# Performance work log

Measured on AMD Instinct MI355X. Metric: run time of the kernel, lower is better.

## Reference

```python
import jax, jax.numpy as jnp
import numpy as np

N = 40000       # nodes
E = 400000      # directed edges (before self-loops)
F_IN = 50       # PPI num_features
HID = 64        # per-head hidden
H = 4           # heads
NCLS = 121      # PPI num_classes
NEG_SLOPE = 0.2


def gat_layer(x, src, dst, W, a_src, a_dst, W_res, b, concat):
    """PyG GATConv: per-edge attention, segment softmax over dst, scatter-add."""
    n = x.shape[0]
    h, c = a_src.shape
    feat = (x @ W).reshape(n, h, c)                       # [N,H,C]
    al_s = (feat * a_src[None]).sum(-1)                   # [N,H]
    al_d = (feat * a_dst[None]).sum(-1)                   # [N,H]
    e = jax.nn.leaky_relu(al_s[src] + al_d[dst], NEG_SLOPE)  # [E,H]
    m = jax.ops.segment_max(e, dst, num_segments=n)       # stable softmax max
    e = jnp.exp(e - m[dst])
    denom = jax.ops.segment_sum(e, dst, num_segments=n)
    w = e / (denom[dst] + 1e-16)                          # [E,H] attention
    msg = feat[src] * w[:, :, None]                       # [E,H,C]
    out = jax.ops.segment_sum(msg, dst, num_segments=n)   # [N,H,C]
    out = out.reshape(n, h * c) if concat else out.mean(axis=1)
    return out + x @ W_res + b                            # residual proj + bias


def setup_inputs() -> dict:
    key = jax.random.key(0)
    ks = jax.random.split(key, 18)
    g = lambda k, shape: jax.random.normal(k, shape, dtype=jnp.float32) * 0.1
    return {
        "x": jax.random.normal(ks[0], (N, F_IN), dtype=jnp.float32),
        "edge_index": jax.random.randint(ks[1], (2, E), 0, N, dtype=jnp.int32),
        "W1": g(ks[2], (F_IN, H * HID)), "a1s": g(ks[3], (H, HID)), "a1d": g(ks[4], (H, HID)),
        "Wr1": g(ks[5], (F_IN, H * HID)), "b1": jnp.zeros((H * HID,), jnp.float32),
        "W2": g(ks[6], (H * HID, H * HID)), "a2s": g(ks[7], (H, HID)), "a2d": g(ks[8], (H, HID)),
        "Wr2": g(ks[9], (H * HID, H * HID)), "b2": jnp.zeros((H * HID,), jnp.float32),
        "W3": g(ks[10], (H * HID, H * NCLS)), "a3s": g(ks[11], (H, NCLS)), "a3d": g(ks[12], (H, NCLS)),
        "Wr3": g(ks[13], (H * HID, NCLS)), "b3": jnp.zeros((NCLS,), jnp.float32),
    }


def reference(x, edge_index, W1, a1s, a1d, Wr1, b1, W2, a2s, a2d, Wr2, b2,
              W3, a3s, a3d, Wr3, b3):
    loop = jnp.arange(N, dtype=edge_index.dtype)          # add_self_loops=True
    src = jnp.concatenate([edge_index[0], loop])
    dst = jnp.concatenate([edge_index[1], loop])
    h = jax.nn.relu(gat_layer(x, src, dst, W1, a1s, a1d, Wr1, b1, True))
    h = jax.nn.relu(gat_layer(h, src, dst, W2, a2s, a2d, Wr2, b2, True))
    return gat_layer(h, src, dst, W3, a3s, a3d, Wr3, b3, False)
```

## Files before the change

kernel.cpp:

```cpp
#include <hip/hip_runtime.h>
#include <hip/hip_bf16.h>


#define NNODES 40000
#define MPAD   40064
#define NEDGES 400000
#define FIN    50
#define NHEAD  4
#define SCANB  157
#define N4     160000

typedef __attribute__((ext_vector_type(8))) short short8;
typedef __attribute__((ext_vector_type(4))) float float4v;
typedef __attribute__((ext_vector_type(2))) float float2v;
typedef __attribute__((ext_vector_type(4))) unsigned short ushort4v;
typedef __attribute__((ext_vector_type(8))) unsigned short ushort8v;
typedef __attribute__((ext_vector_type(2))) unsigned int uint2v;
typedef __attribute__((ext_vector_type(4))) unsigned int uint4v;

__device__ inline unsigned short f2bf(float f) {
    union { float f; unsigned u; } v; v.f = f;
    unsigned r = v.u + 0x7fff + ((v.u >> 16) & 1);
    return (unsigned short)(r >> 16);
}
__device__ inline float bf2f(unsigned short u) {
    union { unsigned u; float f; } v; v.u = ((unsigned)u) << 16; return v.f;
}
__device__ inline float lrelu(float x) { return x >= 0.f ? x : 0.2f * x; }

typedef __attribute__((address_space(3))) unsigned int lds_u32;
typedef __attribute__((address_space(1))) const unsigned int glb_u32;
__device__ __forceinline__ void gl2lds16(const short* g, short* l) {
    __builtin_amdgcn_global_load_lds((glb_u32*)g, (lds_u32*)l, 16, 0, 0);
}

__global__ void hist_kernel(const int* __restrict__ dst, int* __restrict__ counts, int E) {
    int i = blockIdx.x * blockDim.x + threadIdx.x;
    if (i < E) atomicAdd(&counts[dst[i]], 1);
}

__global__ __launch_bounds__(256) void scan_local(const int* __restrict__ counts,
                                                  int* __restrict__ offsets,
                                                  int* __restrict__ partials) {
    __shared__ int sh[256];
    int b = blockIdx.x, t = threadIdx.x, i = b * 256 + t;
    int v = (i < NNODES) ? counts[i] : 0;
    sh[t] = v;
    __syncthreads();
    #pragma unroll
    for (int off = 1; off < 256; off <<= 1) {
        int u = (t >= off) ? sh[t - off] : 0;
        __syncthreads();
        sh[t] += u;
        __syncthreads();
    }
    if (i < NNODES) offsets[i] = sh[t] - v;
    if (t == 255) partials[b] = sh[255];
}

__global__ __launch_bounds__(256) void scan_partials(int* __restrict__ partials,
                                                     int* __restrict__ pexcl) {
    __shared__ int sh[256];
    int t = threadIdx.x;
    int v = (t < SCANB) ? partials[t] : 0;
    sh[t] = v;
    __syncthreads();
    #pragma unroll
    for (int off = 1; off < 256; off <<= 1) {
        int u = (t >= off) ? sh[t - off] : 0;
        __syncthreads();
        sh[t] += u;
        __syncthreads();
    }
    pexcl[t] = sh[t] - v;
}

__global__ __launch_bounds__(256) void scan_carry(int* __restrict__ offsets,
                                                  const int* __restrict__ pexcl) {
    int b = blockIdx.x, i = b * 256 + threadIdx.x;
    if (i < NNODES) offsets[i] += pexcl[b];
}

__global__ void scatter_kernel(const int* __restrict__ src, const int* __restrict__ dst,
                               int* __restrict__ offsets,
                               int* __restrict__ csr_src, int E) {
    int i = blockIdx.x * blockDim.x + threadIdx.x;
    if (i < E) {
        int d = dst[i];
        int pos = atomicAdd(&offsets[d], 1);
        csr_src[pos] = src[i];
    }
}

__global__ void al_combine(float* __restrict__ al4) {
    int i = blockIdx.x * blockDim.x + threadIdx.x;
    if (i >= 80000) return;
    float4v* dst; const float4v* src;
    if (i < 40000) { dst = (float4v*)&al4[2 * N4] + i;            src = (const float4v*)&al4[0] + i; }
    else           { dst = (float4v*)&al4[3 * N4] + (i - 40000);  src = (const float4v*)&al4[N4] + (i - 40000); }
    float4v d = *dst, s0 = *src;
    d.x += s0.x; d.y += s0.y; d.z += s0.z; d.w += s0.w;
    *dst = d;
}

__global__ void convert_x(const float* __restrict__ x, short* __restrict__ xb) {
    int i = blockIdx.x * blockDim.x + threadIdx.x;
    if (i >= MPAD * 64) return;
    int r = i >> 6, k = i & 63;
    float v = (r < NNODES && k < FIN) ? x[r * FIN + k] : 0.f;
    xb[i] = f2bf(v);
}

__global__ void convert_pack1(const float* __restrict__ W1, const float* __restrict__ Wr1,
                              const float* __restrict__ W2, const float* __restrict__ Wr2,
                              short* __restrict__ wc1, short* __restrict__ wc2) {
    int i = blockIdx.x * blockDim.x + threadIdx.x;
    if (i < 32768) {
        const float* W = (i < 16384) ? W1 : Wr1;
        int j = i & 16383;
        int n = j >> 6, k = j & 63;
        wc1[i] = f2bf((k < FIN) ? W[k * 256 + n] : 0.f);
    } else if (i < 163840) {
        int j = (i - 32768) & 65535;
        const float* W = (i < 98304) ? W2 : Wr2;
        int n = j >> 8, k = j & 255;
        wc2[(i - 32768)] = f2bf(W[k * 256 + n]);
    }
}

__global__ void convert_pack2(const float* __restrict__ W3, const float* __restrict__ Wr3,
                              const float* __restrict__ a3s, const float* __restrict__ a3d,
                              short* __restrict__ wc3,
                              float* __restrict__ a3sp, float* __restrict__ a3dp) {
    int i = blockIdx.x * blockDim.x + threadIdx.x;
    if (i < 131072) {
        int j = i >> 8, k = i & 255;
        int h = j >> 7, c = j & 127;
        wc3[i] = f2bf((c < 121) ? W3[k * 484 + h * 121 + c] : 0.f);
    } else if (i < 163840) {
        int j = i - 131072;
        int n = j >> 8, k = j & 255;
        wc3[131072 + j] = f2bf((n < 121) ? Wr3[k * 121 + n] : 0.f);
    } else if (i < 164864) {
        int j = i - 163840;
        int which = j >> 9; int jj = j & 511;
        int h = jj >> 7, c = jj & 127;
        float v = (c < 121) ? (which ? a3d[h * 121 + c] : a3s[h * 121 + c]) : 0.f;
        (which ? a3dp : a3sp)[jj] = v;
    }
}

template<int MODE>
__global__ __launch_bounds__(256) void mfma_gemm_fused(const short* __restrict__ A,
                                                       const short* __restrict__ Bt,
                                                       const float* __restrict__ bias,
                                                       const float* __restrict__ asv,
                                                       const float* __restrict__ adv,
                                                       unsigned short* __restrict__ Fb,
                                                       unsigned short* __restrict__ Rb,
                                                       unsigned int* __restrict__ F8,
                                                       float* __restrict__ out,
                                                       float* __restrict__ al4,
                                                       int Kp) {
    const int NW  = MODE ? 512 : 256;
    const int NCB = MODE ? 5 : 4;
    __shared__ __align__(16) char smem[32768];
    short* As = (short*)smem;
    short* Bs = (short*)(smem + 16384);
    auto Cs = (unsigned short (*)[32][132])smem;
    float* Ls = (float*)smem;

    const int tid = threadIdx.x;
    const int l   = tid & 63;
    const int w   = tid >> 6;
    const int wm  = w >> 1, wn = w & 1;
    const int lrow = l & 15;
    const int lq   = l >> 4;

    const int T = NCB * 313;
    const int flat = blockIdx.y * NCB + blockIdx.x;
    const int q8 = T >> 3, r8 = T & 7;
    const int xcd = flat & 7, sidx = flat >> 3;
    const int wg = (xcd < r8 ? xcd * (q8 + 1) : r8 * (q8 + 1) + (xcd - r8) * q8) + sidx;
    const int row0 = (wg / NCB) * 128;
    const int col0 = (wg % NCB) * 128;

    float4v acc[4][4] = {};

    const int lr_ld = tid >> 3;
    const int lk_ld = (tid & 7) * 8;
    const int nk = Kp >> 6;
    for (int t = 0; t < nk; ++t) {
        const int k0 = t << 6;
        if (t) __syncthreads();
        const size_t abase = (size_t)(row0 + lr_ld) * Kp + k0 + lk_ld;
        const size_t bbase = (size_t)(col0 + lr_ld) * Kp + k0 + lk_ld;
        #pragma unroll
        for (int j = 0; j < 4; ++j) {
            gl2lds16(&A[abase + (size_t)j * 32 * Kp],  &As[j * 2048 + tid * 8]);
            gl2lds16(&Bt[bbase + (size_t)j * 32 * Kp], &Bs[j * 2048 + tid * 8]);
        }
        __syncthreads();
        #pragma unroll
        for (int ks = 0; ks < 2; ++ks) {
            short8 aF[4], bF[4];
            #pragma unroll
            for (int rt = 0; rt < 4; ++rt)
                aF[rt] = *(const short8*)&As[(wm * 64 + rt * 16 + lrow) * 64 + ks * 32 + lq * 8];
            #pragma unroll
            for (int ct = 0; ct < 4; ++ct)
                bF[ct] = *(const short8*)&Bs[(wn * 64 + ct * 16 + lrow) * 64 + ks * 32 + lq * 8];
            #pragma unroll
            for (int rt = 0; rt < 4; ++rt)
                #pragma unroll
                for (int ct = 0; ct < 4; ++ct)
                    acc[rt][ct] = __builtin_amdgcn_mfma_f32_16x16x32_bf16(aF[rt], bF[ct],
                                                                          acc[rt][ct], 0, 0, 0);
        }
    }

    const int colbase = col0 + wn * 64;
    const bool isW = colbase < NW;

    if (isW) {
        const int head = (colbase * NHEAD) / NW;
        const int half = MODE ? ((colbase >> 6) & 1) : 0;
        float* als_o = al4 + (half ? 2 * N4 : 0);
        float* ald_o = als_o + N4;
        float as_c[4], ad_c[4];
        #pragma unroll
        for (int ct = 0; ct < 4; ++ct) {
            int col = colbase + ct * 16 + lrow;
            as_c[ct] = asv[col];
            ad_c[ct] = adv[col];
        }
        #pragma unroll
        for (int rt = 0; rt < 4; ++rt) {
            #pragma unroll
            for (int i = 0; i < 4; ++i) {
                int r = row0 + wm * 64 + rt * 16 + lq * 4 + i;
                float fs = 0.f, fd = 0.f;
                #pragma unroll
                for (int ct = 0; ct < 4; ++ct) {
                    float v = acc[rt][ct][i];
                    fs += v * as_c[ct];
                    fd += v * ad_c[ct];
                }
                #pragma unroll
                for (int o2 = 8; o2; o2 >>= 1) {
                    fs += __shfl_xor(fs, o2, 16);
                    fd += __shfl_xor(fd, o2, 16);
                }
                if (lrow == 0 && r < NNODES) {
                    als_o[r * 4 + head] = fs;
                    ald_o[r * 4 + head] = fd;
                }
            }
        }
    }

    const int rp = tid >> 2, g2 = rp >> 5, rr = rp & 31, qq = tid & 3;

    if (MODE == 1 && col0 >= 512) {
        #pragma unroll
        for (int p = 0; p < 4; ++p) {
            __syncthreads();
            if (wm == (p >> 1)) {
                const int rt0 = (p & 1) * 2;
                #pragma unroll
                for (int rt2 = 0; rt2 < 2; ++rt2) {
                    int rt = rt0 + rt2;
                    #pragma unroll
                    for (int ct = 0; ct < 4; ++ct) {
                        int cl = wn * 64 + ct * 16 + lrow;
                        #pragma unroll
                        for (int i = 0; i < 4; ++i) {
                            int lr = rt2 * 16 + lq * 4 + i;
                            Ls[lr * 132 + cl] = acc[rt][ct][i];
                        }
                    }
                }
            }
            __syncthreads();
            #pragma unroll
            for (int it = 0; it < 16; ++it) {
                int idx = it * 256 + tid;
                int r = idx >> 7, c = idx & 127;
                int grow = row0 + p * 32 + r;
                if (c < 121 && grow < NNODES)
                    out[(size_t)grow * 121 + c] = Ls[r * 132 + c] + bias[c];
            }
        }
        return;
    }

    if (MODE == 1) {
        #pragma unroll
        for (int p = 0; p < 2; ++p) {
            __syncthreads();
            #pragma unroll
            for (int rt2 = 0; rt2 < 2; ++rt2) {
                int rt = p * 2 + rt2;
                #pragma unroll
                for (int ct = 0; ct < 4; ++ct) {
                    int cl = wn * 64 + ct * 16 + lrow;
                    #pragma unroll
                    for (int i = 0; i < 4; ++i) {
                        int lr = rt2 * 16 + lq * 4 + i;
                        Cs[wm][lr][cl] = f2bf(acc[rt][ct][i]);
                    }
                }
            }
            __syncthreads();
            int grow = row0 + g2 * 64 + p * 32 + rr;
            if (grow < NNODES) {
                #pragma unroll
                for (int k = 0; k < 4; ++k) {
                    ushort8v v = *(const ushort8v*)&Cs[g2][rr][qq * 32 + 8 * k];
                    int u0 = 0, u1 = 0;
                    u0 = __builtin_amdgcn_cvt_pk_fp8_f32(bf2f(v[0]), bf2f(v[1]), u0, false);
                    u0 = __builtin_amdgcn_cvt_pk_fp8_f32(bf2f(v[2]), bf2f(v[3]), u0, true);
                    u1 = __builtin_amdgcn_cvt_pk_fp8_f32(bf2f(v[4]), bf2f(v[5]), u1, false);
                    u1 = __builtin_amdgcn_cvt_pk_fp8_f32(bf2f(v[6]), bf2f(v[7]), u1, true);
                    uint2v wv; wv.x = (unsigned)u0; wv.y = (unsigned)u1;
                    *(uint2v*)&F8[(size_t)grow * 128 + (col0 >> 2) + qq * 8 + 2 * k] = wv;
                }
            }
        }
        return;
    }

    const bool isRb = col0 >= 256;
    unsigned short* dest = isRb ? Rb : Fb;
    const int cold = isRb ? col0 - 256 : col0;
    float badd[4] = {0.f, 0.f, 0.f, 0.f};
    if (isRb) {
        #pragma unroll
        for (int ct = 0; ct < 4; ++ct)
            badd[ct] = bias[col0 - 256 + wn * 64 + ct * 16 + lrow];
    }

    #pragma unroll
    for (int p = 0; p < 2; ++p) {
        __syncthreads();
        #pragma unroll
        for (int rt2 = 0; rt2 < 2; ++rt2) {
            int rt = p * 2 + rt2;
            #pragma unroll
            for (int ct = 0; ct < 4; ++ct) {
                int cl = wn * 64 + ct * 16 + lrow;
                #pragma unroll
                for (int i = 0; i < 4; ++i) {
                    int lr = rt2 * 16 + lq * 4 + i;
                    Cs[wm][lr][cl] = f2bf(acc[rt][ct][i] + badd[ct]);
                }
            }
        }
        __syncthreads();
        int grow = row0 + g2 * 64 + p * 32 + rr;
        if (grow < NNODES) {
            #pragma unroll
            for (int k = 0; k < 4; ++k) {
                ushort8v v = *(const ushort8v*)&Cs[g2][rr][qq * 32 + 8 * k];
                *(ushort8v*)&dest[(size_t)grow * 256 + cold + qq * 32 + 8 * k] = v;
            }
        }
    }
}

__global__ __launch_bounds__(256) void attn64_kernel(const unsigned short* __restrict__ featb,
                                                     const float* __restrict__ al4,
                                                     const int* __restrict__ offs,
                                                     const int* __restrict__ csr,
                                                     const unsigned short* __restrict__ Rb,
                                                     unsigned short* __restrict__ outb) {
    int n = blockIdx.x * 4 + (threadIdx.x >> 6);
    int l = threadIdx.x & 63;
    int half = l >> 5, li = l & 31;
    int h = li >> 3;
    int beg = n ? offs[n - 1] : 0;
    int end = offs[n];
    float d0 = al4[N4 + n * 4 + h];

    float a[8] = {};
    float s = 0.f;

    int j = beg + half;
    int sn_n = 0;
    ushort8v u_c = {};
    float al_c = 0.f;
    if (j < end) {
        int sn_c = csr[j];
        u_c = *(const ushort8v*)&featb[(size_t)sn_c * 256 + 8 * li];
        al_c = al4[sn_c * 4 + h];
    }
    if (j + 2 < end) sn_n = csr[j + 2];

    for (; j < end; j += 2) {
        int j2 = j + 2;
        int sn_nn = (j2 + 2 < end) ? csr[j2 + 2] : 0;
        ushort8v u_n = *(const ushort8v*)&featb[(size_t)sn_n * 256 + 8 * li];
        float al_n = al4[sn_n * 4 + h];
        float p_c = __expf(lrelu(al_c + d0));
        s += p_c;
        #pragma unroll
        for (int i = 0; i < 8; ++i) a[i] += p_c * bf2f(u_c[i]);
        u_c = u_n; al_c = al_n; sn_n = sn_nn;
    }
    s += __shfl_xor(s, 32, 64);
    #pragma unroll
    for (int i = 0; i < 8; ++i) a[i] += __shfl_xor(a[i], 32, 64);

    float p0 = __expf(lrelu(al4[n * 4 + h] + d0));
    s += p0;
    {
        ushort8v f = *(const ushort8v*)&featb[(size_t)n * 256 + 8 * li];
        #pragma unroll
        for (int i = 0; i < 8; ++i) a[i] += p0 * bf2f(f[i]);
    }
    if (half == 0) {
        float inv = 1.f / s;
        ushort8v r = *(const ushort8v*)&Rb[(size_t)n * 256 + 8 * li];
        ushort8v o;
        #pragma unroll
        for (int i = 0; i < 8; ++i) o[i] = f2bf(fmaxf(bf2f(r[i]) + a[i] * inv, 0.f));
        *(ushort8v*)&outb[(size_t)n * 256 + 8 * li] = o;
    }
}

__global__ __launch_bounds__(256) void attn121_kernel(const unsigned int* __restrict__ F8,
                                                      const float* __restrict__ al4,
                                                      const int* __restrict__ offs,
                                                      const int* __restrict__ csr,
                                                      float* __restrict__ out) {
    int n = blockIdx.x * 4 + (threadIdx.x >> 6);
    int l = threadIdx.x & 63;
    int half = l >> 5, li = l & 31;
    int h = li >> 3;
    int beg = n ? offs[n - 1] : 0;
    int end = offs[n];
    float dD = al4[3 * N4 + n * 4 + h];

    float a[16] = {};
    float s = 0.f;

    int j = beg + half;
    int sn_n = 0;
    uint4v u_c = {};
    float al_c = 0.f;
    if (j < end) {
        int sn_c = csr[j];
        u_c = *(const uint4v*)&F8[(size_t)sn_c * 128 + 4 * li];
        al_c = al4[2 * N4 + sn_c * 4 + h];
    }
    if (j + 2 < end) sn_n = csr[j + 2];

    for (; j < end; j += 2) {
        int j2 = j + 2;
        int sn_nn = (j2 + 2 < end) ? csr[j2 + 2] : 0;
        uint4v u_n = *(const uint4v*)&F8[(size_t)sn_n * 128 + 4 * li];
        float al_n = al4[2 * N4 + sn_n * 4 + h];
        float p_c = __expf(lrelu(al_c + dD));
        s += p_c;
        #pragma unroll
        for (int k = 0; k < 4; ++k) {
            float2v lo = __builtin_amdgcn_cvt_pk_f32_fp8(u_c[k], false);
            float2v hi = __builtin_amdgcn_cvt_pk_f32_fp8(u_c[k], true);
            a[4 * k + 0] += p_c * lo.x; a[4 * k + 1] += p_c * lo.y;
            a[4 * k + 2] += p_c * hi.x; a[4 * k + 3] += p_c * hi.y;
        }
        u_c = u_n; al_c = al_n; sn_n = sn_nn;
    }
    s += __shfl_xor(s, 32, 64);
    #pragma unroll
    for (int i = 0; i < 16; ++i) a[i] += __shfl_xor(a[i], 32, 64);

    float p0 = __expf(lrelu(al4[2 * N4 + n * 4 + h] + dD));
    s += p0;
    {
        uint4v u = *(const uint4v*)&F8[(size_t)n * 128 + 4 * li];
        #pragma unroll
        for (int k = 0; k < 4; ++k) {
            float2v lo = __builtin_amdgcn_cvt_pk_f32_fp8(u[k], false);
            float2v hi = __builtin_amdgcn_cvt_pk_f32_fp8(u[k], true);
            a[4 * k + 0] += p0 * lo.x; a[4 * k + 1] += p0 * lo.y;
            a[4 * k + 2] += p0 * hi.x; a[4 * k + 3] += p0 * hi.y;
        }
    }
    float inv = 0.25f / s;
    #pragma unroll
    for (int i = 0; i < 16; ++i) {
        a[i] *= inv;
        a[i] += __shfl_xor(a[i], 8, 64);
        a[i] += __shfl_xor(a[i], 16, 64);
    }
    if (l < 8) {
        #pragma unroll
        for (int i = 0; i < 16; ++i) {
            int c = 16 * l + i;
            if (c < 121) out[(size_t)n * 121 + c] += a[i];
        }
    }
}

extern "C" void kernel_launch(void* const* d_in, const int* in_sizes, int n_in,
                              void* d_out, int out_size, void* d_ws, size_t ws_size,
                              hipStream_t stream) {
    const float* x   = (const float*)d_in[0];
    const int* ei    = (const int*)d_in[1];
    const float* W1  = (const float*)d_in[2];
    const float* a1s = (const float*)d_in[3];
    const float* a1d = (const float*)d_in[4];
    const float* Wr1 = (const float*)d_in[5];
    const float* b1  = (const float*)d_in[6];
    const float* W2  = (const float*)d_in[7];
    const float* a2s = (const float*)d_in[8];
    const float* a2d = (const float*)d_in[9];
    const float* Wr2 = (const float*)d_in[10];
    const float* b2  = (const float*)d_in[11];
    const float* W3  = (const float*)d_in[12];
    const float* a3s = (const float*)d_in[13];
    const float* a3d = (const float*)d_in[14];
    const float* Wr3 = (const float*)d_in[15];
    const float* b3  = (const float*)d_in[16];
    float* out = (float*)d_out;

    const int* e_src = ei;
    const int* e_dst = ei + NEDGES;

    char* ws = (char*)d_ws;
    size_t off = 0;
    auto carve = [&](size_t bytes) { void* p = ws + off; off += (bytes + 255) & ~255ull; return p; };
    unsigned short* Fb = (unsigned short*)carve((size_t)MPAD * 256 * 2);
    unsigned short* Rb = (unsigned short*)carve((size_t)MPAD * 256 * 2);
    unsigned short* Hb = (unsigned short*)carve((size_t)MPAD * 256 * 2);
    unsigned int* F8 = (unsigned int*)carve((size_t)NNODES * 128 * 4);
    short* xb   = (short*)carve((size_t)MPAD * 64 * 2);
    short* wc1  = (short*)carve((size_t)512 * 64 * 2);
    short* wc2  = (short*)carve((size_t)512 * 256 * 2);
    short* wc3  = (short*)carve((size_t)640 * 256 * 2);
    float* a3sp = (float*)carve(512 * 4);
    float* a3dp = (float*)carve(512 * 4);
    float* al4  = (float*)carve((size_t)4 * N4 * 4);
    int* csr_src = (int*)carve((size_t)NEDGES * 4);
    int* offsets = (int*)carve(((size_t)NNODES + 4) * 4);
    int* counts  = (int*)carve((size_t)NNODES * 4);
    int* partials = (int*)carve(256 * 4);
    int* pexcl    = (int*)carve(256 * 4);

    const int EB = (NEDGES + 255) / 256;
    dim3 blk(256);

    convert_x<<<(MPAD * 64 + 255) / 256, blk, 0, stream>>>(x, xb);
    convert_pack1<<<(163840 + 255) / 256, blk, 0, stream>>>(W1, Wr1, W2, Wr2, wc1, wc2);
    convert_pack2<<<(164864 + 255) / 256, blk, 0, stream>>>(W3, Wr3, a3s, a3d, wc3, a3sp, a3dp);

    hipMemsetAsync(counts, 0, NNODES * 4, stream);
    hist_kernel<<<EB, blk, 0, stream>>>(e_dst, counts, NEDGES);
    scan_local<<<SCANB, blk, 0, stream>>>(counts, offsets, partials);
    scan_partials<<<1, blk, 0, stream>>>(partials, pexcl);
    scan_carry<<<SCANB, blk, 0, stream>>>(offsets, pexcl);
    scatter_kernel<<<EB, blk, 0, stream>>>(e_src, e_dst, offsets, csr_src, NEDGES);

    mfma_gemm_fused<0><<<dim3(4, 313), blk, 0, stream>>>(xb, wc1, b1, a1s, a1d,
                                                         Fb, Rb, nullptr, nullptr, al4, 64);
    attn64_kernel<<<NNODES / 4, blk, 0, stream>>>(Fb, al4, offsets, csr_src, Rb, Hb);

    mfma_gemm_fused<0><<<dim3(4, 313), blk, 0, stream>>>((short*)Hb, wc2, b2, a2s, a2d,
                                                         Fb, Rb, nullptr, nullptr, al4, 256);
    attn64_kernel<<<NNODES / 4, blk, 0, stream>>>(Fb, al4, offsets, csr_src, Rb, Hb);

    mfma_gemm_fused<1><<<dim3(5, 313), blk, 0, stream>>>((short*)Hb, wc3, b3, a3sp, a3dp,
                                                         nullptr, nullptr, F8, out, al4, 256);
    al_combine<<<313, blk, 0, stream>>>(al4);
    attn121_kernel<<<NNODES / 4, blk, 0, stream>>>(F8, al4, offsets, csr_src, out);
}
```

Baseline: 392.3 us.

## Fuse input conversion and histogram into one kernel; split GEMM LDS for fewer barriers

Merges the x conversion, three weight-packing kernels and the edge histogram into a single launch, which removes several kernel launch gaps. In the GEMM, the epilogue staging buffer Cs gets its own LDS allocation instead of aliasing the A/B tiles. That lets the first barrier before the epilogue writes be dropped. The cost is more LDS per block (about 48KB instead of 32KB), which may reduce occupancy.

```diff
diff --git a/kernel.cpp b/kernel.cpp
--- a/kernel.cpp
+++ b/kernel.cpp
@@ -34,9 +34,57 @@
     __builtin_amdgcn_global_load_lds((glb_u32*)g, (lds_u32*)l, 16, 0, 0);
 }
 
-__global__ void hist_kernel(const int* __restrict__ dst, int* __restrict__ counts, int E) {
+#define R0 (MPAD * 64)
+#define R1 (R0 + 163840)
+#define R2 (R1 + 164864)
+#define R3 (R2 + NEDGES)
+__global__ void init_all(const float* __restrict__ x, short* __restrict__ xb,
+                         const float* __restrict__ W1, const float* __restrict__ Wr1,
+                         const float* __restrict__ W2, const float* __restrict__ Wr2,
+                         short* __restrict__ wc1, short* __restrict__ wc2,
+                         const float* __restrict__ W3, const float* __restrict__ Wr3,
+                         const float* __restrict__ a3s, const float* __restrict__ a3d,
+                         short* __restrict__ wc3,
+                         float* __restrict__ a3sp, float* __restrict__ a3dp,
+                         const int* __restrict__ e_dst, int* __restrict__ counts) {
     int i = blockIdx.x * blockDim.x + threadIdx.x;
-    if (i < E) atomicAdd(&counts[dst[i]], 1);
+    if (i < R0) {
+        int r = i >> 6, k = i & 63;
+        float v = (r < NNODES && k < FIN) ? x[r * FIN + k] : 0.f;
+        xb[i] = f2bf(v);
+    } else if (i < R1) {
+        int j = i - R0;
+        if (j < 32768) {
+            const float* W = (j < 16384) ? W1 : Wr1;
+            int jj = j & 16383;
+            int n = jj >> 6, k = jj & 63;
+            wc1[j] = f2bf((k < FIN) ? W[k * 256 + n] : 0.f);
+        } else {
+            int jj = (j - 32768) & 65535;
+            const float* W = (j < 98304) ? W2 : Wr2;
+            int n = jj >> 8, k = jj & 255;
+            wc2[j - 32768] = f2bf(W[k * 256 + n]);
+        }
+    } else if (i < R2) {
+        int j = i - R1;
+        if (j < 131072) {
+            int jj = j >> 8, k = j & 255;
+            int h = jj >> 7, c = jj & 127;
+            wc3[j] = f2bf((c < 121) ? W3[k * 484 + h * 121 + c] : 0.f);
+        } else if (j < 163840) {
+            int jj = j - 131072;
+            int n = jj >> 8, k = jj & 255;
+            wc3[131072 + jj] = f2bf((n < 121) ? Wr3[k * 121 + n] : 0.f);
+        } else {
+            int jj = j - 163840;
+            int which = jj >> 9; int j2 = jj & 511;
+            int h = j2 >> 7, c = j2 & 127;
+            float v = (c < 121) ? (which ? a3d[h * 121 + c] : a3s[h * 121 + c]) : 0.f;
+            (which ? a3dp : a3sp)[j2] = v;
+        }
+    } else if (i < R3) {
+        atomicAdd(&counts[e_dst[i - R2]], 1);
+    }
 }
 
 __global__ __launch_bounds__(256) void scan_local(const int* __restrict__ counts,
@@ -103,53 +151,6 @@
     *dst = d;
 }
 
-__global__ void convert_x(const float* __restrict__ x, short* __restrict__ xb) {
-    int i = blockIdx.x * blockDim.x + threadIdx.x;
-    if (i >= MPAD * 64) return;
-    int r = i >> 6, k = i & 63;
-    float v = (r < NNODES && k < FIN) ? x[r * FIN + k] : 0.f;
-    xb[i] = f2bf(v);
-}
-
-__global__ void convert_pack1(const float* __restrict__ W1, const float* __restrict__ Wr1,
-                              const float* __restrict__ W2, const float* __restrict__ Wr2,
-                              short* __restrict__ wc1, short* __restrict__ wc2) {
-    int i = blockIdx.x * blockDim.x + threadIdx.x;
-    if (i < 32768) {
-        const float* W = (i < 16384) ? W1 : Wr1;
-        int j = i & 16383;
-        int n = j >> 6, k = j & 63;
-        wc1[i] = f2bf((k < FIN) ? W[k * 256 + n] : 0.f);
-    } else if (i < 163840) {
-        int j = (i - 32768) & 65535;
-        const float* W = (i < 98304) ? W2 : Wr2;
-        int n = j >> 8, k = j & 255;
-        wc2[(i - 32768)] = f2bf(W[k * 256 + n]);
-    }
-}
-
-__global__ void convert_pack2(const float* __restrict__ W3, const float* __restrict__ Wr3,
-                              const float* __restrict__ a3s, const float* __restrict__ a3d,
-                              short* __restrict__ wc3,
-                              float* __restrict__ a3sp, float* __restrict__ a3dp) {
-    int i = blockIdx.x * blockDim.x + threadIdx.x;
-    if (i < 131072) {
-        int j = i >> 8, k = i & 255;
-        int h = j >> 7, c = j & 127;
-        wc3[i] = f2bf((c < 121) ? W3[k * 484 + h * 121 + c] : 0.f);
-    } else if (i < 163840) {
-        int j = i - 131072;
-        int n = j >> 8, k = j & 255;
-        wc3[131072 + j] = f2bf((n < 121) ? Wr3[k * 121 + n] : 0.f);
-    } else if (i < 164864) {
-        int j = i - 163840;
-        int which = j >> 9; int jj = j & 511;
-        int h = jj >> 7, c = jj & 127;
-        float v = (c < 121) ? (which ? a3d[h * 121 + c] : a3s[h * 121 + c]) : 0.f;
-        (which ? a3dp : a3sp)[jj] = v;
-    }
-}
-
 template<int MODE>
 __global__ __launch_bounds__(256) void mfma_gemm_fused(const short* __restrict__ A,
                                                        const short* __restrict__ Bt,
@@ -164,11 +165,10 @@
                                                        int Kp) {
     const int NW  = MODE ? 512 : 256;
     const int NCB = MODE ? 5 : 4;
-    __shared__ __align__(16) char smem[32768];
-    short* As = (short*)smem;
-    short* Bs = (short*)(smem + 16384);
-    auto Cs = (unsigned short (*)[32][132])smem;
-    float* Ls = (float*)smem;
+    __shared__ __align__(16) short AsBs[16384];
+    __shared__ __align__(16) unsigned short Cs[2][32][132];
+    short* As = AsBs;
+    short* Bs = AsBs + 8192;
 
     const int tid = threadIdx.x;
     const int l   = tid & 63;
@@ -262,6 +262,7 @@
     const int rp = tid >> 2, g2 = rp >> 5, rr = rp & 31, qq = tid & 3;
 
     if (MODE == 1 && col0 >= 512) {
+        float* Ls = (float*)AsBs;
         #pragma unroll
         for (int p = 0; p < 4; ++p) {
             __syncthreads();
@@ -297,7 +298,7 @@
     if (MODE == 1) {
         #pragma unroll
         for (int p = 0; p < 2; ++p) {
-            __syncthreads();
+            if (p) __syncthreads();
             #pragma unroll
             for (int rt2 = 0; rt2 < 2; ++rt2) {
                 int rt = p * 2 + rt2;
@@ -342,7 +343,7 @@
 
     #pragma unroll
     for (int p = 0; p < 2; ++p) {
-        __syncthreads();
+        if (p) __syncthreads();
         #pragma unroll
         for (int rt2 = 0; rt2 < 2; ++rt2) {
             int rt = p * 2 + rt2;
@@ -551,12 +552,11 @@
     const int EB = (NEDGES + 255) / 256;
     dim3 blk(256);
 
-    convert_x<<<(MPAD * 64 + 255) / 256, blk, 0, stream>>>(x, xb);
-    convert_pack1<<<(163840 + 255) / 256, blk, 0, stream>>>(W1, Wr1, W2, Wr2, wc1, wc2);
-    convert_pack2<<<(164864 + 255) / 256, blk, 0, stream>>>(W3, Wr3, a3s, a3d, wc3, a3sp, a3dp);
-
     hipMemsetAsync(counts, 0, NNODES * 4, stream);
-    hist_kernel<<<EB, blk, 0, stream>>>(e_dst, counts, NEDGES);
+    init_all<<<(R3 + 255) / 256, blk, 0, stream>>>(x, xb, W1, Wr1, W2, Wr2, wc1, wc2,
+                                                   W3, Wr3, a3s, a3d, wc3, a3sp, a3dp,
+                                                   e_dst, counts);
+
     scan_local<<<SCANB, blk, 0, stream>>>(counts, offsets, partials);
     scan_partials<<<1, blk, 0, stream>>>(partials, pexcl);
     scan_carry<<<SCANB, blk, 0, stream>>>(offsets, pexcl);
```

New measurement: 381.9 us (median of 2 runs). 1.03x faster.
